# Kernel tuning notes

Measured on AMD Instinct MI355X. Metric: run time of the kernel, lower is better.

## Reference

```python
import jax, jax.numpy as jnp
import numpy as np

NUM_OBJ = 512   # batch_size(8) * objects_per_scene(64)
K = 16          # parts per object
N = NUM_OBJ * K # total part nodes = 8192
P = 512         # points per part
E = NUM_OBJ * K * (K - 1)  # 122880 directed intra-object edges


def setup_inputs() -> dict:
    key = jax.random.key(0)
    ks = jax.random.split(key, 16)

    def w(k, shape, fan_in):
        return jax.random.normal(k, shape, jnp.float32) / np.sqrt(fan_in)

    inp = {}
    inp["pcls_arr"] = jax.random.normal(ks[0], (N, P, 6), jnp.float32)
    # PointNetfeat pointwise convs (6->64->128->256), BN affine params
    inp["W1"] = w(ks[1], (6, 64), 6);     inp["b1"] = jnp.zeros(64);  inp["g1"] = jnp.ones(64);  inp["bt1"] = jnp.zeros(64)
    inp["W2"] = w(ks[2], (64, 128), 64);  inp["b2"] = jnp.zeros(128); inp["g2"] = jnp.ones(128); inp["bt2"] = jnp.zeros(128)
    inp["W3"] = w(ks[3], (128, 256), 128); inp["b3"] = jnp.zeros(256); inp["g3"] = jnp.ones(256); inp["bt3"] = jnp.zeros(256)
    # object_embedding Linear(256->256)
    inp["We"] = w(ks[4], (256, 256), 256); inp["be"] = jnp.zeros(256)
    # two GCN layers (256->256->256)
    inp["Wg1"] = w(ks[5], (256, 256), 256); inp["bg1"] = jnp.zeros(256)
    inp["Wg2"] = w(ks[6], (256, 256), 256); inp["bg2"] = jnp.zeros(256)
    # connectivity head: Linear(512->256), Linear(256->256), Linear(256->1)
    inp["Wc1"] = w(ks[7], (512, 256), 512); inp["bc1"] = jnp.zeros(256)
    inp["Wc2"] = w(ks[8], (256, 256), 256); inp["bc2"] = jnp.zeros(256)
    inp["Wc3"] = w(ks[9], (256, 1), 256);   inp["bc3"] = jnp.zeros(1)
    # dense intra-object directed edges (i != j), matching the nested-loop construction
    ii, jj = np.meshgrid(np.arange(K), np.arange(K), indexing="ij")
    m = ii != jj
    i_loc, j_loc = ii[m], jj[m]            # [K*(K-1)] local pair indices, row-major order
    base = (np.arange(NUM_OBJ) * K)[:, None]
    inp["edge_src"] = jnp.asarray((base + i_loc[None, :]).reshape(-1), jnp.int32)
    inp["edge_dst"] = jnp.asarray((base + j_loc[None, :]).reshape(-1), jnp.int32)
    inp["edge_obj"] = jnp.asarray(np.repeat(np.arange(NUM_OBJ), K * (K - 1)), jnp.int32)
    inp["edge_i"]   = jnp.asarray(np.tile(i_loc, NUM_OBJ), jnp.int32)
    inp["edge_j"]   = jnp.asarray(np.tile(j_loc, NUM_OBJ), jnp.int32)
    return inp


def _bn(x, g, bt):
    # eval-mode BatchNorm with running_mean=0, running_var=1 -> per-channel affine
    return x * g + bt


def _gcn_layer(x, W, b, edge_src, edge_dst):
    # GCNConv with self-loops and symmetric deg^{-1/2} normalization
    xw = x @ W                                               # [N, C]
    deg = jax.ops.segment_sum(jnp.ones(E, x.dtype), edge_dst, num_segments=N) + 1.0
    dinv = deg ** -0.5
    norm = dinv[edge_src] * dinv[edge_dst]                   # [E]
    agg = jax.ops.segment_sum(xw[edge_src] * norm[:, None], edge_dst, num_segments=N)
    agg = agg + xw * (1.0 / deg)[:, None]                    # self-loop term
    return agg + b


def reference(pcls_arr, W1, b1, g1, bt1, W2, b2, g2, bt2, W3, b3, g3, bt3,
              We, be, Wg1, bg1, Wg2, bg2, Wc1, bc1, Wc2, bc2, Wc3, bc3,
              edge_src, edge_dst, edge_obj, edge_i, edge_j):
    # PointNetfeat: pointwise MLP over points, max-pool -> [N, 256]
    h = jax.nn.relu(_bn(pcls_arr @ W1 + b1, g1, bt1))        # [N, P, 64]
    h = jax.nn.relu(_bn(h @ W2 + b2, g2, bt2))               # [N, P, 128]
    h = _bn(h @ W3 + b3, g3, bt3)                            # [N, P, 256]
    feat = jnp.max(h, axis=1)                                # [N, 256]
    emb = feat @ We + be                                     # object_embedding

    # MultiGCN: gcn -> relu -> gcn
    x = jax.nn.relu(_gcn_layer(emb, Wg1, bg1, edge_src, edge_dst))
    x = _gcn_layer(x, Wg2, bg2, edge_src, edge_dst)          # [N, 256]

    # gather parent/child embeddings, concat, connectivity MLP, tanh
    pair = jnp.concatenate([x[edge_src], x[edge_dst]], axis=1)  # [E, 512]
    c = jax.nn.relu(pair @ Wc1 + bc1)
    c = jax.nn.relu(c @ Wc2 + bc2)
    c = jnp.tanh((c @ Wc3 + bc3)[:, 0])                      # [E]

    # scatter edge scores into per-object KxK matrices (zero diagonal)
    out = jnp.zeros((NUM_OBJ, K, K), c.dtype).at[edge_obj, edge_i, edge_j].set(c)
    return out
```

## Files before the change

kernel.cpp:

```cpp
#include <hip/hip_runtime.h>
#include <hip/hip_bf16.h>
#include <stdint.h>
#include <stddef.h>


typedef short bf16x8 __attribute__((ext_vector_type(8)));
typedef short bf16x4 __attribute__((ext_vector_type(4)));
typedef float f32x4  __attribute__((ext_vector_type(4)));

#define WT1_OFF   0u
#define WT2_OFF   4096u
#define WT3_OFF   20480u
#define B1F_OFF   86016u
#define B2F_OFF   86272u
#define B3F_OFF   86784u

__device__ __forceinline__ unsigned short f2bf(float f) {
  union { float f; unsigned u; } v; v.f = f;
  unsigned r = v.u + 0x7fffu + ((v.u >> 16) & 1u);
  return (unsigned short)(r >> 16);
}

__device__ __forceinline__ bf16x4 pack_relu4(f32x4 d) {
  __hip_bfloat162 lo = __float22bfloat162_rn(make_float2(fmaxf(d.x, 0.f), fmaxf(d.y, 0.f)));
  __hip_bfloat162 hi = __float22bfloat162_rn(make_float2(fmaxf(d.z, 0.f), fmaxf(d.w, 0.f)));
  union { bf16x4 v; __hip_bfloat162 h[2]; } u;
  u.h[0] = lo; u.h[1] = hi;
  return u.v;
}

__global__ void prep_kernel(
    const float* __restrict__ W1, const float* __restrict__ b1,
    const float* __restrict__ g1, const float* __restrict__ bt1,
    const float* __restrict__ W2, const float* __restrict__ b2,
    const float* __restrict__ g2, const float* __restrict__ bt2,
    const float* __restrict__ W3, const float* __restrict__ b3,
    const float* __restrict__ g3, const float* __restrict__ bt3,
    unsigned char* __restrict__ ws)
{
  unsigned short* wt1 = (unsigned short*)(ws + WT1_OFF);
  unsigned short* wt2 = (unsigned short*)(ws + WT2_OFF);
  unsigned short* wt3 = (unsigned short*)(ws + WT3_OFF);
  float* b1f  = (float*)(ws + B1F_OFF);
  float* b2f  = (float*)(ws + B2F_OFF);
  float* b3f  = (float*)(ws + B3F_OFF);

  int i = blockIdx.x * 256 + threadIdx.x;
  if (i < 2048) { int o = i >> 5, c = i & 31;
    float v = (c < 6) ? W1[c*64 + o] * g1[o]
            : (c == 6 ? (b1[o]*g1[o] + bt1[o]) : 0.f);
    wt1[i] = f2bf(v); return; }
  i -= 2048;
  if (i < 8192) { int o = i >> 6, c = i & 63;
    wt2[i] = f2bf(W2[c*128 + o] * g2[o]); return; }
  i -= 8192;
  if (i < 32768) { int o = i >> 7, c = i & 127;
    wt3[i] = f2bf(W3[c*256 + o] * g3[o]); return; }
  i -= 32768;
  if (i < 64)  { b1f[i] = b1[i]*g1[i] + bt1[i]; return; }
  i -= 64;
  if (i < 128) { b2f[i] = b2[i]*g2[i] + bt2[i]; return; }
  i -= 128;
  if (i < 256) { b3f[i] = b3[i]*g3[i] + bt3[i]; }
}

#define LDSX  0
#define LDSH1 5120
#define LDSH2 14336
#define LDSFS 31744

__global__ __launch_bounds__(512)
__attribute__((amdgpu_waves_per_eu(4, 4)))
void pointnet_fused_kernel(
    const float* __restrict__ pcls, const unsigned char* __restrict__ ws,
    const float* __restrict__ We,  const float* __restrict__ be,
    const float* __restrict__ Wg1, const float* __restrict__ bg1,
    const float* __restrict__ Wg2, const float* __restrict__ bg2,
    const float* __restrict__ Wc1, const float* __restrict__ bc1,
    const float* __restrict__ Wc2, const float* __restrict__ bc2,
    const float* __restrict__ Wc3, const float* __restrict__ bc3,
    float* __restrict__ out)
{
  __shared__ __align__(16) unsigned short lds[32256];

  const unsigned short* wt1 = (const unsigned short*)(ws + WT1_OFF);
  const unsigned short* wt2 = (const unsigned short*)(ws + WT2_OFF);
  const unsigned short* wt3 = (const unsigned short*)(ws + WT3_OFF);
  const float* b2f = (const float*)(ws + B2F_OFF);
  const float* b3f = (const float*)(ws + B3F_OFF);

  const int tid  = threadIdx.x;
  const int w    = tid >> 6;
  const int lane = tid & 63;
  const int l15  = lane & 15;
  const int q    = lane >> 4;
  const int obj  = blockIdx.x;

  const int c1t = w & 3;
  const int ph  = w >> 2;

  const int ct2 = (w & 3) * 2;
  const int pb2 = (w >> 2) * 4;

  bf16x8 af1 = *(const bf16x8*)(wt1 + (c1t*16 + l15)*32 + q*8);
  bf16x8 af2[2][2], af3[2][4];
#pragma unroll
  for (int ct = 0; ct < 2; ++ct)
#pragma unroll
    for (int kf = 0; kf < 2; ++kf)
      af2[ct][kf] = *(const bf16x8*)(wt2 + ((ct2 + ct)*16 + l15)*64 + kf*32 + q*8);
#pragma unroll
  for (int nt = 0; nt < 2; ++nt)
#pragma unroll
    for (int kf = 0; kf < 4; ++kf)
      af3[nt][kf] = *(const bf16x8*)(wt3 + ((2*w + nt)*16 + l15)*128 + kf*32 + q*8);

  f32x4 bs2[2];
#pragma unroll
  for (int ct = 0; ct < 2; ++ct)
    bs2[ct] = *(const f32x4*)(b2f + (ct2 + ct)*16 + q*4);

  const int sv = tid < 384;
  const int sp = tid / 3;
  const int sc = tid % 3;
  unsigned* ldsu = (unsigned*)lds;

  for (int i = tid; i < 5120; i += 512) lds[i] = 0;
  if (tid < 256) ((float*)&lds[LDSFS])[tid] = 0.f;
  __syncthreads();
  if (tid < 128) lds[LDSX + tid*40 + 6] = 0x3F80;

  const float* pbase = pcls + (size_t)obj * 49152;
  if (sv) {
    const float2 pv = *(const float2*)(pbase + 2*tid);
    ldsu[sp*20 + sc] = (unsigned)f2bf(pv.x) | ((unsigned)f2bf(pv.y) << 16);
  }
  __syncthreads();

  f32x4 macc[2];
#pragma unroll
  for (int nt = 0; nt < 2; ++nt)
    macc[nt] = (f32x4){-3e38f, -3e38f, -3e38f, -3e38f};

#pragma unroll
  for (int i = 0; i < 4; ++i) {
    const int pt = ph*4 + i;
    bf16x8 b = *(const bf16x8*)(&lds[LDSX + (pt*16 + l15)*40 + q*8]);
    f32x4 d = {0.f, 0.f, 0.f, 0.f};
    d = __builtin_amdgcn_mfma_f32_16x16x32_bf16(af1, b, d, 0, 0, 0);
    *(bf16x4*)(&lds[LDSH1 + (pt*16 + l15)*72 + c1t*16 + q*4]) = pack_relu4(d);
  }
  __syncthreads();

  for (int cg = 0; cg < 64; ++cg) {
    const int havenext = (cg < 63);

    float2 pv;
    if (havenext && sv)
      pv = *(const float2*)(pbase + (cg + 1)*768 + 2*tid);
#pragma unroll
    for (int pt = 0; pt < 4; ++pt) {
      const int ptt = pb2 + pt;
      bf16x8 b0  = *(const bf16x8*)(&lds[LDSH1 + (ptt*16 + l15)*72 + q*8]);
      bf16x8 b1v = *(const bf16x8*)(&lds[LDSH1 + (ptt*16 + l15)*72 + 32 + q*8]);
#pragma unroll
      for (int ct = 0; ct < 2; ++ct) {
        f32x4 d = bs2[ct];
        d = __builtin_amdgcn_mfma_f32_16x16x32_bf16(af2[ct][0], b0,  d, 0, 0, 0);
        d = __builtin_amdgcn_mfma_f32_16x16x32_bf16(af2[ct][1], b1v, d, 0, 0, 0);
        *(bf16x4*)(&lds[LDSH2 + (ptt*16 + l15)*136 + (ct2 + ct)*16 + q*4]) = pack_relu4(d);
      }
    }
    if (havenext && sv)
      ldsu[sp*20 + sc] = (unsigned)f2bf(pv.x) | ((unsigned)f2bf(pv.y) << 16);
    __syncthreads();

    if (havenext) {
#pragma unroll
      for (int i = 0; i < 4; ++i) {
        const int pt = ph*4 + i;
        bf16x8 b = *(const bf16x8*)(&lds[LDSX + (pt*16 + l15)*40 + q*8]);
        f32x4 d = {0.f, 0.f, 0.f, 0.f};
        d = __builtin_amdgcn_mfma_f32_16x16x32_bf16(af1, b, d, 0, 0, 0);
        *(bf16x4*)(&lds[LDSH1 + (pt*16 + l15)*72 + c1t*16 + q*4]) = pack_relu4(d);
      }
    }
#pragma unroll
    for (int pt = 0; pt < 8; ++pt) {
      bf16x8 b[4];
#pragma unroll
      for (int kf = 0; kf < 4; ++kf)
        b[kf] = *(const bf16x8*)(&lds[LDSH2 + (pt*16 + l15)*136 + kf*32 + q*8]);
#pragma unroll
      for (int nt = 0; nt < 2; ++nt) {
        f32x4 d = {0.f, 0.f, 0.f, 0.f};
#pragma unroll
        for (int kf = 0; kf < 4; ++kf)
          d = __builtin_amdgcn_mfma_f32_16x16x32_bf16(af3[nt][kf], b[kf], d, 0, 0, 0);
#pragma unroll
        for (int r = 0; r < 4; ++r)
          macc[nt][r] = fmaxf(macc[nt][r], d[r]);
      }
    }
    if ((cg & 3) == 3) {
      float* fsacc = (float*)&lds[LDSFS];
#pragma unroll
      for (int nt = 0; nt < 2; ++nt) {
#pragma unroll
        for (int r = 0; r < 4; ++r) {
          float v = macc[nt][r];
          v = fmaxf(v, __shfl_xor(v, 1));
          v = fmaxf(v, __shfl_xor(v, 2));
          v = fmaxf(v, __shfl_xor(v, 4));
          v = fmaxf(v, __shfl_xor(v, 8));
          if (l15 == 0) fsacc[(2*w + nt)*16 + q*4 + r] += v;
        }
        macc[nt] = (f32x4){-3e38f, -3e38f, -3e38f, -3e38f};
      }
    }
    __syncthreads();
  }

  float* fls  = (float*)&lds[0];
  float* fs   = (float*)&lds[LDSFS];
  float* bA   = fls;
  float* bB   = fls + 256;
  float* part = fls + 512;
  float* redv = fls + 1024;

  if (tid < 256) fs[tid] += 16.f * b3f[tid];
  __syncthreads();

  const int tt = tid & 255, hh = tid >> 8;
  const int cb = hh * 128;
  float a;

  a = 0.f;
#pragma unroll 8
  for (int c = 0; c < 128; ++c) a += fs[cb + c] * We[(cb + c)*256 + tt];
  part[hh*256 + tt] = a;
  __syncthreads();
  if (hh == 0) bA[tt] = part[tt] + part[256 + tt] + 16.f * be[tt];
  __syncthreads();

  a = 0.f;
#pragma unroll 8
  for (int c = 0; c < 128; ++c) a += bA[cb + c] * Wg1[(cb + c)*256 + tt];
  part[hh*256 + tt] = a;
  __syncthreads();
  if (hh == 0) bB[tt] = fmaxf((part[tt] + part[256 + tt]) * 0.0625f + bg1[tt], 0.f);
  __syncthreads();

  a = 0.f;
#pragma unroll 8
  for (int c = 0; c < 128; ++c) a += bB[cb + c] * Wg2[(cb + c)*256 + tt];
  part[hh*256 + tt] = a;
  __syncthreads();
  if (hh == 0) bA[tt] = part[tt] + part[256 + tt] + bg2[tt];
  __syncthreads();

  a = 0.f;
#pragma unroll 8
  for (int c = 0; c < 128; ++c) {
    const float xv = bA[cb + c];
    a += xv * Wc1[(cb + c)*256 + tt];
    a += xv * Wc1[(cb + c + 256)*256 + tt];
  }
  part[hh*256 + tt] = a;
  __syncthreads();
  if (hh == 0) bB[tt] = fmaxf(part[tt] + part[256 + tt] + bc1[tt], 0.f);
  __syncthreads();

  a = 0.f;
#pragma unroll 8
  for (int c = 0; c < 128; ++c) a += bB[cb + c] * Wc2[(cb + c)*256 + tt];
  part[hh*256 + tt] = a;
  __syncthreads();
  if (hh == 0) bA[tt] = fmaxf(part[tt] + part[256 + tt] + bc2[tt], 0.f);
  __syncthreads();

  float prod = (hh == 0) ? bA[tt] * Wc3[tt] : 0.f;
#pragma unroll
  for (int off = 1; off < 64; off <<= 1) prod += __shfl_xor(prod, off);
  if (lane == 0) redv[w] = prod;
  __syncthreads();
  if (tid == 0) redv[0] = tanhf(redv[0] + redv[1] + redv[2] + redv[3] + bc3[0]);
  __syncthreads();
  const float cv = redv[0];
  if (hh == 0)
    out[obj*256 + tt] = ((tt >> 4) == (tt & 15)) ? 0.f : cv;
}

extern "C" void kernel_launch(void* const* d_in, const int* in_sizes, int n_in,
                              void* d_out, int out_size, void* d_ws, size_t ws_size,
                              hipStream_t stream) {
  const float* pcls = (const float*)d_in[0];
  const float* W1 = (const float*)d_in[1];  const float* b1 = (const float*)d_in[2];
  const float* g1 = (const float*)d_in[3];  const float* bt1 = (const float*)d_in[4];
  const float* W2 = (const float*)d_in[5];  const float* b2 = (const float*)d_in[6];
  const float* g2 = (const float*)d_in[7];  const float* bt2 = (const float*)d_in[8];
  const float* W3 = (const float*)d_in[9];  const float* b3 = (const float*)d_in[10];
  const float* g3 = (const float*)d_in[11]; const float* bt3 = (const float*)d_in[12];
  const float* We = (const float*)d_in[13]; const float* be = (const float*)d_in[14];
  const float* Wg1 = (const float*)d_in[15]; const float* bg1 = (const float*)d_in[16];
  const float* Wg2 = (const float*)d_in[17]; const float* bg2 = (const float*)d_in[18];
  const float* Wc1 = (const float*)d_in[19]; const float* bc1 = (const float*)d_in[20];
  const float* Wc2 = (const float*)d_in[21]; const float* bc2 = (const float*)d_in[22];
  const float* Wc3 = (const float*)d_in[23]; const float* bc3 = (const float*)d_in[24];
  unsigned char* ws = (unsigned char*)d_ws;
  float* out = (float*)d_out;

  prep_kernel<<<170, 256, 0, stream>>>(W1, b1, g1, bt1, W2, b2, g2, bt2,
                                       W3, b3, g3, bt3, ws);
  pointnet_fused_kernel<<<512, 512, 0, stream>>>(
      pcls, ws, We, be, Wg1, bg1, Wg2, bg2, Wc1, bc1, Wc2, bc2, Wc3, bc3, out);
}
```

Measured before the change: 482.4 us.

## Double per-iteration point chunk and retile layer-3 to reuse B fragments across eight channel tiles

Each loop iteration now processes 256 points instead of 128, halving the number of iterations and barriers. Layer-3 work is retiled so each wave holds eight channel-tile weight fragments and reuses each loaded H2 fragment across all of them, which cuts LDS reads per MFMA. The per-part max reduction now goes through an LDS partial-max buffer rather than per-wave accumulation. LDS use doubles and occupancy drops from 4 to 2 waves per EU, with much higher register pressure from af3[8][4] and macc[8].

```diff
diff --git a/kernel.cpp b/kernel.cpp
--- a/kernel.cpp
+++ b/kernel.cpp
@@ -19,6 +19,12 @@
   union { float f; unsigned u; } v; v.f = f;
   unsigned r = v.u + 0x7fffu + ((v.u >> 16) & 1u);
   return (unsigned short)(r >> 16);
+}
+
+__device__ __forceinline__ unsigned pack2bf(float a, float b) {
+  __hip_bfloat162 h = __float22bfloat162_rn(make_float2(a, b));
+  union { __hip_bfloat162 h; unsigned u; } u; u.h = h;
+  return u.u;
 }
 
 __device__ __forceinline__ bf16x4 pack_relu4(f32x4 d) {
@@ -65,12 +71,13 @@
 }
 
 #define LDSX  0
-#define LDSH1 5120
-#define LDSH2 14336
-#define LDSFS 31744
+#define LDSH1 8192
+#define LDSH2 26624
+#define LDSFS 61440
+#define LDSPM 61952
 
 __global__ __launch_bounds__(512)
-__attribute__((amdgpu_waves_per_eu(4, 4)))
+__attribute__((amdgpu_waves_per_eu(2, 2)))
 void pointnet_fused_kernel(
     const float* __restrict__ pcls, const unsigned char* __restrict__ ws,
     const float* __restrict__ We,  const float* __restrict__ be,
@@ -81,7 +88,7 @@
     const float* __restrict__ Wc3, const float* __restrict__ bc3,
     float* __restrict__ out)
 {
-  __shared__ __align__(16) unsigned short lds[32256];
+  __shared__ __align__(16) unsigned short lds[64000];
 
   const unsigned short* wt1 = (const unsigned short*)(ws + WT1_OFF);
   const unsigned short* wt2 = (const unsigned short*)(ws + WT2_OFF);
@@ -98,22 +105,23 @@
 
   const int c1t = w & 3;
   const int ph  = w >> 2;
-
   const int ct2 = (w & 3) * 2;
-  const int pb2 = (w >> 2) * 4;
+  const int pb2 = (w >> 2) * 8;
+  const int cg3 = w & 1;
+  const int pg  = w >> 1;
 
   bf16x8 af1 = *(const bf16x8*)(wt1 + (c1t*16 + l15)*32 + q*8);
-  bf16x8 af2[2][2], af3[2][4];
+  bf16x8 af2[2][2], af3[8][4];
 #pragma unroll
   for (int ct = 0; ct < 2; ++ct)
 #pragma unroll
     for (int kf = 0; kf < 2; ++kf)
       af2[ct][kf] = *(const bf16x8*)(wt2 + ((ct2 + ct)*16 + l15)*64 + kf*32 + q*8);
 #pragma unroll
-  for (int nt = 0; nt < 2; ++nt)
+  for (int ct = 0; ct < 8; ++ct)
 #pragma unroll
     for (int kf = 0; kf < 4; ++kf)
-      af3[nt][kf] = *(const bf16x8*)(wt3 + ((2*w + nt)*16 + l15)*128 + kf*32 + q*8);
+      af3[ct][kf] = *(const bf16x8*)(wt3 + ((cg3*8 + ct)*16 + l15)*128 + kf*32 + q*8);
 
   f32x4 bs2[2];
 #pragma unroll
@@ -121,45 +129,56 @@
     bs2[ct] = *(const f32x4*)(b2f + (ct2 + ct)*16 + q*4);
 
   const int sv = tid < 384;
-  const int sp = tid / 3;
-  const int sc = tid % 3;
+  const int e0 = 4*tid, e2 = 4*tid + 2;
+  const int r0 = e0 / 6, c0 = (e0 % 6) >> 1;
+  const int r1 = e2 / 6, c1 = (e2 % 6) >> 1;
   unsigned* ldsu = (unsigned*)lds;
-
-  for (int i = tid; i < 5120; i += 512) lds[i] = 0;
+  const int d0a = r0*16 + c0;
+  const int d1a = r1*16 + c1;
+
+  for (int i = tid; i < 4096; i += 512) ldsu[i] = 0;
   if (tid < 256) ((float*)&lds[LDSFS])[tid] = 0.f;
   __syncthreads();
-  if (tid < 128) lds[LDSX + tid*40 + 6] = 0x3F80;
+  if (tid < 256) lds[LDSX + tid*32 + 6] = 0x3F80;
 
   const float* pbase = pcls + (size_t)obj * 49152;
   if (sv) {
-    const float2 pv = *(const float2*)(pbase + 2*tid);
-    ldsu[sp*20 + sc] = (unsigned)f2bf(pv.x) | ((unsigned)f2bf(pv.y) << 16);
-  }
-  __syncthreads();
-
-  f32x4 macc[2];
-#pragma unroll
-  for (int nt = 0; nt < 2; ++nt)
-    macc[nt] = (f32x4){-3e38f, -3e38f, -3e38f, -3e38f};
-
-#pragma unroll
-  for (int i = 0; i < 4; ++i) {
-    const int pt = ph*4 + i;
-    bf16x8 b = *(const bf16x8*)(&lds[LDSX + (pt*16 + l15)*40 + q*8]);
+    const float4 g = *(const float4*)(pbase + 4*tid);
+    ldsu[d0a] = pack2bf(g.x, g.y);
+    ldsu[d1a] = pack2bf(g.z, g.w);
+  }
+  __syncthreads();
+
+  f32x4 macc[8];
+#pragma unroll
+  for (int ct = 0; ct < 8; ++ct)
+    macc[ct] = (f32x4){-3e38f, -3e38f, -3e38f, -3e38f};
+
+#pragma unroll
+  for (int i = 0; i < 8; ++i) {
+    const int pt = ph*8 + i;
+    bf16x8 b = *(const bf16x8*)(&lds[LDSX + (pt*16 + l15)*32 + q*8]);
     f32x4 d = {0.f, 0.f, 0.f, 0.f};
     d = __builtin_amdgcn_mfma_f32_16x16x32_bf16(af1, b, d, 0, 0, 0);
     *(bf16x4*)(&lds[LDSH1 + (pt*16 + l15)*72 + c1t*16 + q*4]) = pack_relu4(d);
   }
   __syncthreads();
 
-  for (int cg = 0; cg < 64; ++cg) {
-    const int havenext = (cg < 63);
-
-    float2 pv;
+  for (int cg = 0; cg < 32; ++cg) {
+    const int havenext = (cg < 31);
+
+    float4 g;
     if (havenext && sv)
-      pv = *(const float2*)(pbase + (cg + 1)*768 + 2*tid);
-#pragma unroll
-    for (int pt = 0; pt < 4; ++pt) {
+      g = *(const float4*)(pbase + (cg + 1)*1536 + 4*tid);
+
+    if (cg > 0 && !(cg & 1) && tid < 256) {
+      float* pm = (float*)&lds[LDSPM];
+      float* fsacc = (float*)&lds[LDSFS];
+      fsacc[tid] += fmaxf(fmaxf(pm[tid], pm[256 + tid]),
+                          fmaxf(pm[512 + tid], pm[768 + tid]));
+    }
+#pragma unroll
+    for (int pt = 0; pt < 8; ++pt) {
       const int ptt = pb2 + pt;
       bf16x8 b0  = *(const bf16x8*)(&lds[LDSH1 + (ptt*16 + l15)*72 + q*8]);
       bf16x8 b1v = *(const bf16x8*)(&lds[LDSH1 + (ptt*16 + l15)*72 + 32 + q*8]);
@@ -171,55 +190,70 @@
         *(bf16x4*)(&lds[LDSH2 + (ptt*16 + l15)*136 + (ct2 + ct)*16 + q*4]) = pack_relu4(d);
       }
     }
-    if (havenext && sv)
-      ldsu[sp*20 + sc] = (unsigned)f2bf(pv.x) | ((unsigned)f2bf(pv.y) << 16);
+    if (havenext && sv) {
+      ldsu[d0a] = pack2bf(g.x, g.y);
+      ldsu[d1a] = pack2bf(g.z, g.w);
+    }
     __syncthreads();
 
     if (havenext) {
 #pragma unroll
-      for (int i = 0; i < 4; ++i) {
-        const int pt = ph*4 + i;
-        bf16x8 b = *(const bf16x8*)(&lds[LDSX + (pt*16 + l15)*40 + q*8]);
+      for (int i = 0; i < 8; ++i) {
+        const int pt = ph*8 + i;
+        bf16x8 b = *(const bf16x8*)(&lds[LDSX + (pt*16 + l15)*32 + q*8]);
         f32x4 d = {0.f, 0.f, 0.f, 0.f};
         d = __builtin_amdgcn_mfma_f32_16x16x32_bf16(af1, b, d, 0, 0, 0);
         *(bf16x4*)(&lds[LDSH1 + (pt*16 + l15)*72 + c1t*16 + q*4]) = pack_relu4(d);
       }
     }
 #pragma unroll
-    for (int pt = 0; pt < 8; ++pt) {
+    for (int pt = 0; pt < 4; ++pt) {
+      const int ptt = pg*4 + pt;
       bf16x8 b[4];
 #pragma unroll
       for (int kf = 0; kf < 4; ++kf)
-        b[kf] = *(const bf16x8*)(&lds[LDSH2 + (pt*16 + l15)*136 + kf*32 + q*8]);
-#pragma unroll
-      for (int nt = 0; nt < 2; ++nt) {
+        b[kf] = *(const bf16x8*)(&lds[LDSH2 + (ptt*16 + l15)*136 + kf*32 + q*8]);
+#pragma unroll
+      for (int ct = 0; ct < 8; ++ct) {
         f32x4 d = {0.f, 0.f, 0.f, 0.f};
 #pragma unroll
         for (int kf = 0; kf < 4; ++kf)
-          d = __builtin_amdgcn_mfma_f32_16x16x32_bf16(af3[nt][kf], b[kf], d, 0, 0, 0);
+          d = __builtin_amdgcn_mfma_f32_16x16x32_bf16(af3[ct][kf], b[kf], d, 0, 0, 0);
 #pragma unroll
         for (int r = 0; r < 4; ++r)
-          macc[nt][r] = fmaxf(macc[nt][r], d[r]);
+          macc[ct][r] = fmaxf(macc[ct][r], d[r]);
       }
     }
-    if ((cg & 3) == 3) {
-      float* fsacc = (float*)&lds[LDSFS];
-#pragma unroll
-      for (int nt = 0; nt < 2; ++nt) {
+    if (cg & 1) {
+      float* pm = (float*)&lds[LDSPM];
+#pragma unroll
+      for (int ct = 0; ct < 8; ++ct) {
+        f32x4 v = macc[ct];
 #pragma unroll
         for (int r = 0; r < 4; ++r) {
-          float v = macc[nt][r];
-          v = fmaxf(v, __shfl_xor(v, 1));
-          v = fmaxf(v, __shfl_xor(v, 2));
-          v = fmaxf(v, __shfl_xor(v, 4));
-          v = fmaxf(v, __shfl_xor(v, 8));
-          if (l15 == 0) fsacc[(2*w + nt)*16 + q*4 + r] += v;
+          float x = v[r];
+          x = fmaxf(x, __shfl_xor(x, 1));
+          x = fmaxf(x, __shfl_xor(x, 2));
+          x = fmaxf(x, __shfl_xor(x, 4));
+          x = fmaxf(x, __shfl_xor(x, 8));
+          v[r] = x;
         }
-        macc[nt] = (f32x4){-3e38f, -3e38f, -3e38f, -3e38f};
+        if (l15 == 0)
+          *(f32x4*)(pm + pg*256 + cg3*128 + ct*16 + q*4) = v;
+        macc[ct] = (f32x4){-3e38f, -3e38f, -3e38f, -3e38f};
       }
     }
     __syncthreads();
   }
+
+  if (tid < 256) {
+    float* pm = (float*)&lds[LDSPM];
+    float* fsacc = (float*)&lds[LDSFS];
+    fsacc[tid] += fmaxf(fmaxf(pm[tid], pm[256 + tid]),
+                        fmaxf(pm[512 + tid], pm[768 + tid]));
+    fsacc[tid] += 16.f * b3f[tid];
+  }
+  __syncthreads();
 
   float* fls  = (float*)&lds[0];
   float* fs   = (float*)&lds[LDSFS];
@@ -227,9 +261,6 @@
   float* bB   = fls + 256;
   float* part = fls + 512;
   float* redv = fls + 1024;
-
-  if (tid < 256) fs[tid] += 16.f * b3f[tid];
-  __syncthreads();
 
   const int tt = tid & 255, hh = tid >> 8;
   const int cb = hh * 128;
```

After: 852.3 us. 1.77x slower.

## Re-tile layer-2/3 MFMA work split across waves with two-stage partial max

Applied to the files above, without the earlier changes.

Changes how the 8 waves split the conv2 and conv3 MFMA work. For conv2, each wave now owns one 16-channel tile over all 8 point tiles instead of two channel tiles over 4 point tiles. For conv3, each wave owns 4 channel tiles over 4 point tiles instead of 2 channel tiles over all 8. Because two point-groups now cover the same channels, partial maxima go to a new LDS buffer and are combined into the feature sum at the start of the next group and after the loop. This changes B-operand reuse and LDS read traffic, at the cost of more weight registers (af3 grows to 16 fragments) and slightly more LDS.

```diff
diff --git a/kernel.cpp b/kernel.cpp
--- a/kernel.cpp
+++ b/kernel.cpp
@@ -68,6 +68,7 @@
 #define LDSH1 5120
 #define LDSH2 14336
 #define LDSFS 31744
+#define LDSPM 32256
 
 __global__ __launch_bounds__(512)
 __attribute__((amdgpu_waves_per_eu(4, 4)))
@@ -81,7 +82,7 @@
     const float* __restrict__ Wc3, const float* __restrict__ bc3,
     float* __restrict__ out)
 {
-  __shared__ __align__(16) unsigned short lds[32256];
+  __shared__ __align__(16) unsigned short lds[33280];
 
   const unsigned short* wt1 = (const unsigned short*)(ws + WT1_OFF);
   const unsigned short* wt2 = (const unsigned short*)(ws + WT2_OFF);
@@ -98,27 +99,21 @@
 
   const int c1t = w & 3;
   const int ph  = w >> 2;
-
-  const int ct2 = (w & 3) * 2;
-  const int pb2 = (w >> 2) * 4;
+  const int cq  = w & 3;
+  const int pg  = w >> 2;
 
   bf16x8 af1 = *(const bf16x8*)(wt1 + (c1t*16 + l15)*32 + q*8);
-  bf16x8 af2[2][2], af3[2][4];
-#pragma unroll
-  for (int ct = 0; ct < 2; ++ct)
-#pragma unroll
-    for (int kf = 0; kf < 2; ++kf)
-      af2[ct][kf] = *(const bf16x8*)(wt2 + ((ct2 + ct)*16 + l15)*64 + kf*32 + q*8);
-#pragma unroll
-  for (int nt = 0; nt < 2; ++nt)
+  bf16x8 af2[2], af3[4][4];
+#pragma unroll
+  for (int kf = 0; kf < 2; ++kf)
+    af2[kf] = *(const bf16x8*)(wt2 + (w*16 + l15)*64 + kf*32 + q*8);
+#pragma unroll
+  for (int ct = 0; ct < 4; ++ct)
 #pragma unroll
     for (int kf = 0; kf < 4; ++kf)
-      af3[nt][kf] = *(const bf16x8*)(wt3 + ((2*w + nt)*16 + l15)*128 + kf*32 + q*8);
-
-  f32x4 bs2[2];
-#pragma unroll
-  for (int ct = 0; ct < 2; ++ct)
-    bs2[ct] = *(const f32x4*)(b2f + (ct2 + ct)*16 + q*4);
+      af3[ct][kf] = *(const bf16x8*)(wt3 + ((cq*4 + ct)*16 + l15)*128 + kf*32 + q*8);
+
+  const f32x4 bias2 = *(const f32x4*)(b2f + w*16 + q*4);
 
   const int sv = tid < 384;
   const int sp = tid / 3;
@@ -137,10 +132,10 @@
   }
   __syncthreads();
 
-  f32x4 macc[2];
-#pragma unroll
-  for (int nt = 0; nt < 2; ++nt)
-    macc[nt] = (f32x4){-3e38f, -3e38f, -3e38f, -3e38f};
+  f32x4 macc[4];
+#pragma unroll
+  for (int ct = 0; ct < 4; ++ct)
+    macc[ct] = (f32x4){-3e38f, -3e38f, -3e38f, -3e38f};
 
 #pragma unroll
   for (int i = 0; i < 4; ++i) {
@@ -158,18 +153,20 @@
     float2 pv;
     if (havenext && sv)
       pv = *(const float2*)(pbase + (cg + 1)*768 + 2*tid);
-#pragma unroll
-    for (int pt = 0; pt < 4; ++pt) {
-      const int ptt = pb2 + pt;
-      bf16x8 b0  = *(const bf16x8*)(&lds[LDSH1 + (ptt*16 + l15)*72 + q*8]);
-      bf16x8 b1v = *(const bf16x8*)(&lds[LDSH1 + (ptt*16 + l15)*72 + 32 + q*8]);
-#pragma unroll
-      for (int ct = 0; ct < 2; ++ct) {
-        f32x4 d = bs2[ct];
-        d = __builtin_amdgcn_mfma_f32_16x16x32_bf16(af2[ct][0], b0,  d, 0, 0, 0);
-        d = __builtin_amdgcn_mfma_f32_16x16x32_bf16(af2[ct][1], b1v, d, 0, 0, 0);
-        *(bf16x4*)(&lds[LDSH2 + (ptt*16 + l15)*136 + (ct2 + ct)*16 + q*4]) = pack_relu4(d);
-      }
+
+    if ((cg & 3) == 0 && cg > 0 && tid < 256) {
+      float* pm = (float*)&lds[LDSPM];
+      float* fsacc = (float*)&lds[LDSFS];
+      fsacc[tid] += fmaxf(pm[tid], pm[256 + tid]);
+    }
+#pragma unroll
+    for (int pt = 0; pt < 8; ++pt) {
+      bf16x8 b0  = *(const bf16x8*)(&lds[LDSH1 + (pt*16 + l15)*72 + q*8]);
+      bf16x8 b1v = *(const bf16x8*)(&lds[LDSH1 + (pt*16 + l15)*72 + 32 + q*8]);
+      f32x4 d = bias2;
+      d = __builtin_amdgcn_mfma_f32_16x16x32_bf16(af2[0], b0,  d, 0, 0, 0);
+      d = __builtin_amdgcn_mfma_f32_16x16x32_bf16(af2[1], b1v, d, 0, 0, 0);
+      *(bf16x4*)(&lds[LDSH2 + (pt*16 + l15)*136 + w*16 + q*4]) = pack_relu4(d);
     }
     if (havenext && sv)
       ldsu[sp*20 + sc] = (unsigned)f2bf(pv.x) | ((unsigned)f2bf(pv.y) << 16);
@@ -186,40 +183,52 @@
       }
     }
 #pragma unroll
-    for (int pt = 0; pt < 8; ++pt) {
+    for (int pt = 0; pt < 4; ++pt) {
+      const int ptt = pg*4 + pt;
       bf16x8 b[4];
 #pragma unroll
       for (int kf = 0; kf < 4; ++kf)
-        b[kf] = *(const bf16x8*)(&lds[LDSH2 + (pt*16 + l15)*136 + kf*32 + q*8]);
-#pragma unroll
-      for (int nt = 0; nt < 2; ++nt) {
+        b[kf] = *(const bf16x8*)(&lds[LDSH2 + (ptt*16 + l15)*136 + kf*32 + q*8]);
+#pragma unroll
+      for (int ct = 0; ct < 4; ++ct) {
         f32x4 d = {0.f, 0.f, 0.f, 0.f};
 #pragma unroll
         for (int kf = 0; kf < 4; ++kf)
-          d = __builtin_amdgcn_mfma_f32_16x16x32_bf16(af3[nt][kf], b[kf], d, 0, 0, 0);
+          d = __builtin_amdgcn_mfma_f32_16x16x32_bf16(af3[ct][kf], b[kf], d, 0, 0, 0);
 #pragma unroll
         for (int r = 0; r < 4; ++r)
-          macc[nt][r] = fmaxf(macc[nt][r], d[r]);
+          macc[ct][r] = fmaxf(macc[ct][r], d[r]);
       }
     }
     if ((cg & 3) == 3) {
-      float* fsacc = (float*)&lds[LDSFS];
-#pragma unroll
-      for (int nt = 0; nt < 2; ++nt) {
+      float* pm = (float*)&lds[LDSPM];
+#pragma unroll
+      for (int ct = 0; ct < 4; ++ct) {
+        f32x4 v = macc[ct];
 #pragma unroll
         for (int r = 0; r < 4; ++r) {
-          float v = macc[nt][r];
-          v = fmaxf(v, __shfl_xor(v, 1));
-          v = fmaxf(v, __shfl_xor(v, 2));
-          v = fmaxf(v, __shfl_xor(v, 4));
-          v = fmaxf(v, __shfl_xor(v, 8));
-          if (l15 == 0) fsacc[(2*w + nt)*16 + q*4 + r] += v;
+          float x = v[r];
+          x = fmaxf(x, __shfl_xor(x, 1));
+          x = fmaxf(x, __shfl_xor(x, 2));
+          x = fmaxf(x, __shfl_xor(x, 4));
+          x = fmaxf(x, __shfl_xor(x, 8));
+          v[r] = x;
         }
-        macc[nt] = (f32x4){-3e38f, -3e38f, -3e38f, -3e38f};
+        if (l15 == 0)
+          *(f32x4*)(pm + pg*256 + (cq*4 + ct)*16 + q*4) = v;
+        macc[ct] = (f32x4){-3e38f, -3e38f, -3e38f, -3e38f};
       }
     }
     __syncthreads();
   }
+
+  if (tid < 256) {
+    float* pm = (float*)&lds[LDSPM];
+    float* fsacc = (float*)&lds[LDSFS];
+    fsacc[tid] += fmaxf(pm[tid], pm[256 + tid]);
+    fsacc[tid] += 16.f * b3f[tid];
+  }
+  __syncthreads();
 
   float* fls  = (float*)&lds[0];
   float* fs   = (float*)&lds[LDSFS];
@@ -227,9 +236,6 @@
   float* bB   = fls + 256;
   float* part = fls + 512;
   float* redv = fls + 1024;
-
-  if (tid < 256) fs[tid] += 16.f * b3f[tid];
-  __syncthreads();
 
   const int tt = tid & 255, hh = tid >> 8;
   const int cb = hh * 128;
```

Result: slower. 1.371 ms (+184.1%).

## Prefetch point chunks two iterations ahead and regroup layer-1 MFMA work per wave

Applied to the files above, without the earlier changes.

The global load of the next point chunk is now issued two iterations ahead into a register, and its bf16 conversion and LDS write happen at the start of the iteration instead of after the layer-2 MFMAs. This hides more of the global memory latency behind compute. Layer-1 work is also redistributed so each wave computes two channel tiles for two point tiles, reusing each LDS B-fragment load across two MFMAs. It adds registers (two af1 fragments, an sacc array that is declared but unused) and may raise register pressure.

```diff
diff --git a/kernel.cpp b/kernel.cpp
--- a/kernel.cpp
+++ b/kernel.cpp
@@ -96,14 +96,16 @@
   const int q    = lane >> 4;
   const int obj  = blockIdx.x;
 
-  const int c1t = w & 3;
-  const int ph  = w >> 2;
+  const int c1g = w & 1;
+  const int p1g = w >> 1;
 
   const int ct2 = (w & 3) * 2;
   const int pb2 = (w >> 2) * 4;
 
-  bf16x8 af1 = *(const bf16x8*)(wt1 + (c1t*16 + l15)*32 + q*8);
-  bf16x8 af2[2][2], af3[2][4];
+  bf16x8 af1[2], af2[2][2], af3[2][4];
+#pragma unroll
+  for (int ct = 0; ct < 2; ++ct)
+    af1[ct] = *(const bf16x8*)(wt1 + ((c1g*2 + ct)*16 + l15)*32 + q*8);
 #pragma unroll
   for (int ct = 0; ct < 2; ++ct)
 #pragma unroll
@@ -135,29 +137,41 @@
     const float2 pv = *(const float2*)(pbase + 2*tid);
     ldsu[sp*20 + sc] = (unsigned)f2bf(pv.x) | ((unsigned)f2bf(pv.y) << 16);
   }
+  float2 pvh;
+  if (sv) pvh = *(const float2*)(pbase + 768 + 2*tid);
   __syncthreads();
 
   f32x4 macc[2];
-#pragma unroll
-  for (int nt = 0; nt < 2; ++nt)
+  float sacc[2][4];
+#pragma unroll
+  for (int nt = 0; nt < 2; ++nt) {
     macc[nt] = (f32x4){-3e38f, -3e38f, -3e38f, -3e38f};
-
-#pragma unroll
-  for (int i = 0; i < 4; ++i) {
-    const int pt = ph*4 + i;
+#pragma unroll
+    for (int r = 0; r < 4; ++r) sacc[nt][r] = 0.f;
+  }
+
+#pragma unroll
+  for (int i = 0; i < 2; ++i) {
+    const int pt = p1g*2 + i;
     bf16x8 b = *(const bf16x8*)(&lds[LDSX + (pt*16 + l15)*40 + q*8]);
-    f32x4 d = {0.f, 0.f, 0.f, 0.f};
-    d = __builtin_amdgcn_mfma_f32_16x16x32_bf16(af1, b, d, 0, 0, 0);
-    *(bf16x4*)(&lds[LDSH1 + (pt*16 + l15)*72 + c1t*16 + q*4]) = pack_relu4(d);
+#pragma unroll
+    for (int ct = 0; ct < 2; ++ct) {
+      f32x4 d = {0.f, 0.f, 0.f, 0.f};
+      d = __builtin_amdgcn_mfma_f32_16x16x32_bf16(af1[ct], b, d, 0, 0, 0);
+      *(bf16x4*)(&lds[LDSH1 + (pt*16 + l15)*72 + (c1g*2 + ct)*16 + q*4]) = pack_relu4(d);
+    }
   }
   __syncthreads();
 
   for (int cg = 0; cg < 64; ++cg) {
-    const int havenext = (cg < 63);
-
-    float2 pv;
-    if (havenext && sv)
-      pv = *(const float2*)(pbase + (cg + 1)*768 + 2*tid);
+    const int havewrite = (cg < 63);
+    const int haveload  = (cg < 62);
+
+    if (havewrite && sv)
+      ldsu[sp*20 + sc] = (unsigned)f2bf(pvh.x) | ((unsigned)f2bf(pvh.y) << 16);
+    if (haveload && sv)
+      pvh = *(const float2*)(pbase + (cg + 2)*768 + 2*tid);
+
 #pragma unroll
     for (int pt = 0; pt < 4; ++pt) {
       const int ptt = pb2 + pt;
@@ -171,18 +185,19 @@
         *(bf16x4*)(&lds[LDSH2 + (ptt*16 + l15)*136 + (ct2 + ct)*16 + q*4]) = pack_relu4(d);
       }
     }
-    if (havenext && sv)
-      ldsu[sp*20 + sc] = (unsigned)f2bf(pv.x) | ((unsigned)f2bf(pv.y) << 16);
     __syncthreads();
 
-    if (havenext) {
-#pragma unroll
-      for (int i = 0; i < 4; ++i) {
-        const int pt = ph*4 + i;
+    if (havewrite) {
+#pragma unroll
+      for (int i = 0; i < 2; ++i) {
+        const int pt = p1g*2 + i;
         bf16x8 b = *(const bf16x8*)(&lds[LDSX + (pt*16 + l15)*40 + q*8]);
-        f32x4 d = {0.f, 0.f, 0.f, 0.f};
-        d = __builtin_amdgcn_mfma_f32_16x16x32_bf16(af1, b, d, 0, 0, 0);
-        *(bf16x4*)(&lds[LDSH1 + (pt*16 + l15)*72 + c1t*16 + q*4]) = pack_relu4(d);
+#pragma unroll
+        for (int ct = 0; ct < 2; ++ct) {
+          f32x4 d = {0.f, 0.f, 0.f, 0.f};
+          d = __builtin_amdgcn_mfma_f32_16x16x32_bf16(af1[ct], b, d, 0, 0, 0);
+          *(bf16x4*)(&lds[LDSH1 + (pt*16 + l15)*72 + (c1g*2 + ct)*16 + q*4]) = pack_relu4(d);
+        }
       }
     }
 #pragma unroll
```

New measurement: 490.0 us. No clear change (+1.6%).
